# Kernel optimization log

Measured on AMD Instinct MI355X. Metric: run time of the kernel, lower is better.

## Reference

```python
import jax, jax.numpy as jnp
import numpy as np

EPS = 1e-5

def _bn(x, p):
    # eval-mode BatchNorm over the last (channel) axis; p = [gamma, beta, mean, var]
    g, b, m, v = p[0], p[1], p[2], p[3]
    return (x - m) * jax.lax.rsqrt(v + EPS) * g + b

def _mk_bn(key, c):
    kg, kb, km, kv = jax.random.split(key, 4)
    return jnp.stack([
        jax.random.uniform(kg, (c,), minval=0.5, maxval=1.5),
        jax.random.normal(kb, (c,)) * 0.1,
        jax.random.normal(km, (c,)) * 0.1,
        jax.random.uniform(kv, (c,), minval=0.5, maxval=1.5),
    ]).astype(jnp.float32)

def setup_inputs() -> dict:
    key = jax.random.key(0)
    ks = jax.random.split(key, 12)
    B, N, K = 2, 65536, 16
    IN_CH, OUT_CH = 32, 128
    D = IN_CH + 3            # 35
    C16 = OUT_CH // 16       # 8
    C4 = OUT_CH // 4         # 32
    G = 1                    # num_group
    feats = jax.random.normal(ks[0], (B, N, D), dtype=jnp.float32)
    idx = jax.random.randint(ks[1], (B, N, K), 0, N, dtype=jnp.int64)
    s = lambda fi, fo: (2.0 / fi) ** 0.5
    return {
        "features": feats,
        "idx": idx,
        "point_W": jax.random.normal(ks[2], (10, C16), dtype=jnp.float32) * s(10, C16),
        "point_bn": _mk_bn(ks[3], C16),
        "eta_W": jax.random.normal(ks[4], (IN_CH, C16), dtype=jnp.float32) * s(IN_CH, C16),
        "eta_bn": _mk_bn(ks[5], C16),
        "mu_W": jax.random.normal(ks[6], (IN_CH, C16), dtype=jnp.float32) * s(IN_CH, C16),
        "mu_bn": _mk_bn(ks[7], C16),
        "gamma_W": jax.random.normal(ks[8], (D, C4), dtype=jnp.float32) * s(D, C4),
        "gamma_bn": _mk_bn(ks[9], C4),
        "map_W": jax.random.normal(ks[10], (3 * C16, G), dtype=jnp.float32) * s(3 * C16, G),
        "map_bn": _mk_bn(ks[10], G),
        "fc_W": jax.random.normal(ks[11], (C4, OUT_CH), dtype=jnp.float32) * s(C4, OUT_CH),
    }

def reference(features, idx, point_W, point_bn, eta_W, eta_bn, mu_W, mu_bn,
              gamma_W, gamma_bn, map_W, map_bn, fc_W):
    # features: [B,N,D] (D = 3 xyz + in_channel), idx: [B,N,K] kNN indices
    nbr = jax.vmap(lambda f, i: f[i])(features, idx)     # [B,N,K,D] gather
    pn = nbr[..., :3]                                    # neighbor xyz
    pnf = nbr[..., 3:]                                   # neighbor feats
    feat = features[..., 3:]                             # center feats [B,N,Cin]
    p = features[:, :, None, :3]                         # center xyz, bcast over K
    diff = p - pn
    point = jnp.concatenate([
        jnp.sum(diff * diff, axis=-1, keepdims=True),
        jnp.broadcast_to(p, pn.shape), pn, diff,
    ], axis=-1)                                          # [B,N,K,10]
    point = jax.nn.relu(_bn(point @ point_W, point_bn))  # [B,N,K,C16]
    eta = _bn((feat @ eta_W)[:, :, None, :], eta_bn)     # [B,N,1,C16] (repeat over K)
    mu = _bn(pnf @ mu_W, mu_bn)                          # [B,N,K,C16]
    feature = jnp.concatenate([jnp.broadcast_to(eta, mu.shape), mu], axis=-1)  # concat mode
    feature = jnp.concatenate([point, feature], axis=-1)                       # [B,N,K,3*C16]
    feature = jax.nn.relu(_bn(feature @ map_W, map_bn))  # [B,N,K,G]
    gam = _bn(nbr @ gamma_W, gamma_bn)                   # [B,N,K,C4]
    rep = gam.shape[-1] // feature.shape[-1]             # out/4 / num_group
    feature = jnp.tile(feature, (1, 1, 1, rep))          # channel repeat
    out = jnp.max(feature * gam, axis=2)                 # max over neighbors -> [B,N,C4]
    return out @ fc_W                                    # [B,N,out_channel]
```

## Files before the change

### kernel.cpp

```cpp
#include <hip/hip_runtime.h>
#include <hip/hip_fp16.h>
#include <math.h>

#define N_PTS   65536
#define BATCH   2
#define TOTAL   (BATCH * N_PTS)
#define NPACK   24
#define CPACK   12
#define EPSB    1e-5f

typedef short short8 __attribute__((ext_vector_type(8)));
typedef float f32x4 __attribute__((ext_vector_type(4)));

static __device__ inline short f2bf(float x) {
    union { float f; unsigned u; } c; c.f = x;
    unsigned r = c.u + 0x7FFF + ((c.u >> 16) & 1);
    return (short)(r >> 16);
}
static __device__ inline unsigned pk_mul(unsigned a, unsigned b) {
    unsigned r; asm("v_pk_mul_f16 %0, %1, %2" : "=v"(r) : "v"(a), "v"(b)); return r;
}
static __device__ inline unsigned pk_max(unsigned a, unsigned b) {
    unsigned r; asm("v_pk_max_f16 %0, %1, %2" : "=v"(r) : "v"(a), "v"(b)); return r;
}

__global__ __launch_bounds__(256) void k1_precompute(
    const float* __restrict__ feats,
    const float* __restrict__ pW,
    const float* __restrict__ pBN,
    const float* __restrict__ eW,
    const float* __restrict__ eBN,
    const float* __restrict__ mW,
    const float* __restrict__ mBN,
    const float* __restrict__ gW,
    const float* __restrict__ gBN,
    const float* __restrict__ mapW,
    float* __restrict__ packN,
    float* __restrict__ packC)
{
    __shared__ float sF[256 * 35];

    const int tid = threadIdx.x;
    const int base = blockIdx.x * 256;

#pragma unroll
    for (int t = 0; t < 35; ++t)
        sF[t * 256 + tid] = feats[(size_t)base * 35 + t * 256 + tid];
    __syncthreads();

    const float* f = sF + tid * 35;
    const float x = f[0], y = f[1], z = f[2];
    const float pp = x * x + y * y + z * z;

    float G[32];
#pragma unroll
    for (int q = 0; q < 32; ++q) G[q] = 0.f;
#pragma unroll 4
    for (int d = 0; d < 35; ++d) {
        const float fd = f[d];
        const float4* w4 = (const float4*)(gW + d * 32);
#pragma unroll
        for (int q4 = 0; q4 < 8; ++q4) {
            const float4 w = w4[q4];
            G[q4 * 4 + 0] = fmaf(fd, w.x, G[q4 * 4 + 0]);
            G[q4 * 4 + 1] = fmaf(fd, w.y, G[q4 * 4 + 1]);
            G[q4 * 4 + 2] = fmaf(fd, w.z, G[q4 * 4 + 2]);
            G[q4 * 4 + 3] = fmaf(fd, w.w, G[q4 * 4 + 3]);
        }
    }
#pragma unroll
    for (int q = 0; q < 32; ++q) {
        const float g = gBN[q], b = gBN[32 + q], m = gBN[64 + q], v = gBN[96 + q];
        const float s = g / sqrtf(v + EPSB);
        G[q] = fmaf(G[q], s, b - m * s);
    }

    float eta[8], mu[8];
#pragma unroll
    for (int q = 0; q < 8; ++q) { eta[q] = 0.f; mu[q] = 0.f; }
#pragma unroll 4
    for (int i = 0; i < 32; ++i) {
        const float fi = f[3 + i];
        const float4* e4 = (const float4*)(eW + i * 8);
        const float4* m4 = (const float4*)(mW + i * 8);
#pragma unroll
        for (int h = 0; h < 2; ++h) {
            const float4 we = e4[h], wm = m4[h];
            eta[h * 4 + 0] = fmaf(fi, we.x, eta[h * 4 + 0]);
            eta[h * 4 + 1] = fmaf(fi, we.y, eta[h * 4 + 1]);
            eta[h * 4 + 2] = fmaf(fi, we.z, eta[h * 4 + 2]);
            eta[h * 4 + 3] = fmaf(fi, we.w, eta[h * 4 + 3]);
            mu[h * 4 + 0] = fmaf(fi, wm.x, mu[h * 4 + 0]);
            mu[h * 4 + 1] = fmaf(fi, wm.y, mu[h * 4 + 1]);
            mu[h * 4 + 2] = fmaf(fi, wm.z, mu[h * 4 + 2]);
            mu[h * 4 + 3] = fmaf(fi, wm.w, mu[h * 4 + 3]);
        }
    }
    float etadot = 0.f, Mdot = 0.f;
#pragma unroll
    for (int q = 0; q < 8; ++q) {
        const float ge = eBN[q], be = eBN[8 + q], me = eBN[16 + q], ve = eBN[24 + q];
        const float se = ge / sqrtf(ve + EPSB);
        etadot = fmaf(fmaf(eta[q], se, be - me * se), mapW[8 + q], etadot);
        const float gm = mBN[q], bm = mBN[8 + q], mm = mBN[16 + q], vm = mBN[24 + q];
        const float sm = gm / sqrtf(vm + EPSB);
        Mdot = fmaf(fmaf(mu[q], sm, bm - mm * sm), mapW[16 + q], Mdot);
    }

    float Bnp[8], Ap[8];
#pragma unroll
    for (int q = 0; q < 8; ++q) {
        const float pw0 = pW[q];
        const float g = pBN[q], b = pBN[8 + q], m = pBN[16 + q], v = pBN[24 + q];
        const float s = g / sqrtf(v + EPSB);
        const float t = b - m * s;
        const float Braw = pp * pw0
            + x * (pW[32 + q] - pW[56 + q])
            + y * (pW[40 + q] - pW[64 + q])
            + z * (pW[48 + q] - pW[72 + q]);
        const float Araw = pp * pw0
            + x * (pW[8 + q]  + pW[56 + q])
            + y * (pW[16 + q] + pW[64 + q])
            + z * (pW[24 + q] + pW[72 + q]);
        Bnp[q] = Braw * s;
        Ap[q]  = fmaf(Araw, s, t);
    }

    const int j = base + tid;
    float4* PN = (float4*)(packN + (size_t)j * NPACK);
    PN[0] = make_float4(x, y, z, Mdot);
    {
        float4 b4;
        __half2* hb = (__half2*)&b4;
        hb[0] = __floats2half2_rn(Bnp[0], Bnp[1]);
        hb[1] = __floats2half2_rn(Bnp[2], Bnp[3]);
        hb[2] = __floats2half2_rn(Bnp[4], Bnp[5]);
        hb[3] = __floats2half2_rn(Bnp[6], Bnp[7]);
        PN[1] = b4;
    }
#pragma unroll
    for (int q = 0; q < 4; ++q) {
        float4 g4;
        __half2* hg = (__half2*)&g4;
        hg[0] = __floats2half2_rn(G[q * 8 + 0], G[q * 8 + 1]);
        hg[1] = __floats2half2_rn(G[q * 8 + 2], G[q * 8 + 3]);
        hg[2] = __floats2half2_rn(G[q * 8 + 4], G[q * 8 + 5]);
        hg[3] = __floats2half2_rn(G[q * 8 + 6], G[q * 8 + 7]);
        PN[2 + q] = g4;
    }

    float4* PC = (float4*)(packC + (size_t)j * CPACK);
    PC[0] = make_float4(x, y, z, etadot);
    PC[1] = make_float4(Ap[0], Ap[1], Ap[2], Ap[3]);
    PC[2] = make_float4(Ap[4], Ap[5], Ap[6], Ap[7]);
}

__global__ __launch_bounds__(256) void k2_aggregate_fc(
    const int* __restrict__ idx,
    const float* __restrict__ packN,
    const float* __restrict__ packC,
    const float* __restrict__ pW,
    const float* __restrict__ pBN,
    const float* __restrict__ mapW,
    const float* __restrict__ mapBN,
    const float* __restrict__ fcW,
    float* __restrict__ out)
{
    __shared__ __align__(16) unsigned short sPool[32 * 40];

    const int tid  = threadIdx.x;
    const int cl   = tid >> 3;
    const int ks   = tid & 7;
    const int cbase = blockIdx.x * 32;
    const int c    = cbase + cl;
    const int lane = tid & 63;
    const int w    = tid >> 6;
    const int lm   = lane & 15, lq = lane >> 4;

    short8 bfrag[2];
#pragma unroll
    for (int ntj = 0; ntj < 2; ++ntj) {
        const int nt = 2 * w + ntj;
#pragma unroll
        for (int j = 0; j < 8; ++j)
            bfrag[ntj][j] = f2bf(fcW[(8 * lq + j) * 128 + nt * 16 + lm]);
    }

    float ms, mt;
    {
        const float g = mapBN[0], b = mapBN[1], m = mapBN[2], v = mapBN[3];
        ms = g / sqrtf(v + EPSB);
        mt = b - m * ms;
    }
    float W0p[8], mW0[8];
#pragma unroll
    for (int q = 0; q < 8; ++q) {
        const float g = pBN[q], v = pBN[24 + q];
        const float s = g / sqrtf(v + EPSB);
        W0p[q] = 2.f * pW[q] * s;
        mW0[q] = mapW[q];
    }

    const float4* PC = (const float4*)(packC + (size_t)c * CPACK);
    const float4 c0 = PC[0], c1 = PC[1], c2 = PC[2];
    const float px = c0.x, py = c0.y, pz = c0.z, etadot = c0.w;
    const float Ap[8] = { c1.x, c1.y, c1.z, c1.w, c2.x, c2.y, c2.z, c2.w };

    const int2 ib2 = ((const int2*)idx)[c * 8 + ks];
    const int nbr[2] = { ib2.x, ib2.y };
    const int bbase = c & ~(N_PTS - 1);

    unsigned o16[16];
#pragma unroll
    for (int q = 0; q < 16; ++q) o16[q] = 0xFC00FC00u;

#pragma unroll
    for (int k = 0; k < 2; ++k) {
        const int gj = bbase + nbr[k];
        const float4* P = (const float4*)(packN + (size_t)gj * NPACK);
        const float4 h  = P[0];
        const float4 b4 = P[1];
        const float4 g0 = P[2], g1 = P[3], g2 = P[4], g3 = P[5];

        const float dot3 = px * h.x + py * h.y + pz * h.z;
        const __half2* hb = (const __half2*)&b4;
        float pd = 0.f;
#pragma unroll
        for (int q = 0; q < 4; ++q) {
            const float2 bn2 = __half22float2(hb[q]);
            const float u0 = Ap[2 * q]     + bn2.x - dot3 * W0p[2 * q];
            const float u1 = Ap[2 * q + 1] + bn2.y - dot3 * W0p[2 * q + 1];
            pd = fmaf(fmaxf(u0, 0.f), mW0[2 * q], pd);
            pd = fmaf(fmaxf(u1, 0.f), mW0[2 * q + 1], pd);
        }
        float s = fmaf(pd + etadot + h.w, ms, mt);
        s = fmaxf(s, 0.f);

        const unsigned short su = __half_as_ushort(__float2half_rn(s));
        const unsigned s2 = (unsigned)su * 0x10001u;

        const float4 gs[4] = { g0, g1, g2, g3 };
#pragma unroll
        for (int q = 0; q < 4; ++q) {
            const unsigned* hg = (const unsigned*)&gs[q];
#pragma unroll
            for (int r = 0; r < 4; ++r)
                o16[q * 4 + r] = pk_max(o16[q * 4 + r], pk_mul(s2, hg[r]));
        }
    }

#pragma unroll
    for (int q = 0; q < 16; ++q) {
        unsigned v = o16[q];
        v = pk_max(v, (unsigned)__shfl_xor((int)v, 1));
        v = pk_max(v, (unsigned)__shfl_xor((int)v, 2));
        v = pk_max(v, (unsigned)__shfl_xor((int)v, 4));
        o16[q] = v;
    }

    {
        const unsigned v0 = o16[2 * ks], v1 = o16[2 * ks + 1];
        const float c0f = __half2float(__ushort_as_half((unsigned short)(v0 & 0xffff)));
        const float c1f = __half2float(__ushort_as_half((unsigned short)(v0 >> 16)));
        const float c2f = __half2float(__ushort_as_half((unsigned short)(v1 & 0xffff)));
        const float c3f = __half2float(__ushort_as_half((unsigned short)(v1 >> 16)));
        uint2 pk;
        pk.x = (unsigned short)f2bf(c0f) | ((unsigned)(unsigned short)f2bf(c1f) << 16);
        pk.y = (unsigned short)f2bf(c2f) | ((unsigned)(unsigned short)f2bf(c3f) << 16);
        *(uint2*)(sPool + cl * 40 + ks * 4) = pk;
    }
    __syncthreads();

    f32x4 acc[2][2];
#pragma unroll
    for (int a = 0; a < 2; ++a)
#pragma unroll
        for (int b = 0; b < 2; ++b)
            acc[a][b] = (f32x4){0.f, 0.f, 0.f, 0.f};

#pragma unroll
    for (int mtile = 0; mtile < 2; ++mtile) {
        const short8 afrag = *(const short8*)(sPool + (mtile * 16 + lm) * 40 + lq * 8);
#pragma unroll
        for (int ntj = 0; ntj < 2; ++ntj)
            acc[mtile][ntj] = __builtin_amdgcn_mfma_f32_16x16x32_bf16(
                afrag, bfrag[ntj], acc[mtile][ntj], 0, 0, 0);
    }

#pragma unroll
    for (int mtile = 0; mtile < 2; ++mtile)
#pragma unroll
        for (int ntj = 0; ntj < 2; ++ntj) {
            const int nt = 2 * w + ntj;
#pragma unroll
            for (int r = 0; r < 4; ++r)
                out[(size_t)(cbase + mtile * 16 + lq * 4 + r) * 128 + nt * 16 + lm] =
                    acc[mtile][ntj][r];
        }
}

extern "C" void kernel_launch(void* const* d_in, const int* in_sizes, int n_in,
                              void* d_out, int out_size, void* d_ws, size_t ws_size,
                              hipStream_t stream) {
    const float* feats    = (const float*)d_in[0];
    const int*   idx      = (const int*)  d_in[1];
    const float* point_W  = (const float*)d_in[2];
    const float* point_bn = (const float*)d_in[3];
    const float* eta_W    = (const float*)d_in[4];
    const float* eta_bn   = (const float*)d_in[5];
    const float* mu_W     = (const float*)d_in[6];
    const float* mu_bn    = (const float*)d_in[7];
    const float* gamma_W  = (const float*)d_in[8];
    const float* gamma_bn = (const float*)d_in[9];
    const float* map_W    = (const float*)d_in[10];
    const float* map_bn   = (const float*)d_in[11];
    const float* fc_W     = (const float*)d_in[12];
    float* out = (float*)d_out;

    float* packN  = (float*)d_ws;
    float* packC  = packN + (size_t)TOTAL * NPACK;

    hipLaunchKernelGGL(k1_precompute, dim3(TOTAL / 256), dim3(256), 0, stream,
                       feats, point_W, point_bn, eta_W, eta_bn, mu_W, mu_bn,
                       gamma_W, gamma_bn, map_W, packN, packC);
    hipLaunchKernelGGL(k2_aggregate_fc, dim3(TOTAL / 32), dim3(256), 0, stream,
                       idx, packN, packC, point_W, point_bn, map_W, map_bn,
                       fc_W, out);
}
```

Baseline: 177.0 us.

## Quantize gathered gamma to int8, pack neighbor record in 64B, remap blocks per XCD

Shrinks the per-neighbor packed record from 96 to 64 bytes. It stores xyz and the point terms as fp16 and the 32 gamma values as per-point-scaled int8, which cuts gather traffic in the aggregation kernel. It also remaps block IDs so each XCD works on one batch half, giving the random gathers better L2 locality. It switches the pooled values and fc MFMA from bf16 to fp16 to drop conversions, uses nontemporal output stores, and stages weights in LDS in the precompute kernel. Risks include int8 quantization error, fp16 xyz precision loss, and extra dequantization ALU work.

```diff
diff --git a/kernel.cpp b/kernel.cpp
--- a/kernel.cpp
+++ b/kernel.cpp
@@ -5,20 +5,19 @@
 #define N_PTS   65536
 #define BATCH   2
 #define TOTAL   (BATCH * N_PTS)
-#define NPACK   24
+#define NPACK_DW 16
 #define CPACK   12
 #define EPSB    1e-5f
 
-typedef short short8 __attribute__((ext_vector_type(8)));
-typedef float f32x4 __attribute__((ext_vector_type(4)));
-
-static __device__ inline short f2bf(float x) {
-    union { float f; unsigned u; } c; c.f = x;
-    unsigned r = c.u + 0x7FFF + ((c.u >> 16) & 1);
-    return (short)(r >> 16);
-}
-static __device__ inline unsigned pk_mul(unsigned a, unsigned b) {
-    unsigned r; asm("v_pk_mul_f16 %0, %1, %2" : "=v"(r) : "v"(a), "v"(b)); return r;
+typedef float  f32x4  __attribute__((ext_vector_type(4)));
+typedef _Float16 f16x8 __attribute__((ext_vector_type(8)));
+
+static __device__ inline unsigned h2u(float a, float b) {
+    __half2 h = __floats2half2_rn(a, b);
+    union { __half2 h; unsigned u; } cv; cv.h = h; return cv.u;
+}
+static __device__ inline float2 u2f2(unsigned u) {
+    union { unsigned u; __half2 h; } cv; cv.u = u; return __half22float2(cv.h);
 }
 static __device__ inline unsigned pk_max(unsigned a, unsigned b) {
     unsigned r; asm("v_pk_max_f16 %0, %1, %2" : "=v"(r) : "v"(a), "v"(b)); return r;
@@ -35,14 +34,19 @@
     const float* __restrict__ gW,
     const float* __restrict__ gBN,
     const float* __restrict__ mapW,
-    float* __restrict__ packN,
+    unsigned* __restrict__ packN,
     float* __restrict__ packC)
 {
+    __shared__ float sG[35 * 32];
+    __shared__ float sE[32 * 8];
+    __shared__ float sM[32 * 8];
     __shared__ float sF[256 * 35];
 
     const int tid = threadIdx.x;
     const int base = blockIdx.x * 256;
 
+    for (int i = tid; i < 35 * 32; i += 256) sG[i] = gW[i];
+    sE[tid] = eW[tid]; sM[tid] = mW[tid];
 #pragma unroll
     for (int t = 0; t < 35; ++t)
         sF[t * 256 + tid] = feats[(size_t)base * 35 + t * 256 + tid];
@@ -58,7 +62,7 @@
 #pragma unroll 4
     for (int d = 0; d < 35; ++d) {
         const float fd = f[d];
-        const float4* w4 = (const float4*)(gW + d * 32);
+        const float4* w4 = (const float4*)(sG + d * 32);
 #pragma unroll
         for (int q4 = 0; q4 < 8; ++q4) {
             const float4 w = w4[q4];
@@ -81,8 +85,8 @@
 #pragma unroll 4
     for (int i = 0; i < 32; ++i) {
         const float fi = f[3 + i];
-        const float4* e4 = (const float4*)(eW + i * 8);
-        const float4* m4 = (const float4*)(mW + i * 8);
+        const float4* e4 = (const float4*)(sE + i * 8);
+        const float4* m4 = (const float4*)(sM + i * 8);
 #pragma unroll
         for (int h = 0; h < 2; ++h) {
             const float4 we = e4[h], wm = m4[h];
@@ -127,27 +131,28 @@
     }
 
     const int j = base + tid;
-    float4* PN = (float4*)(packN + (size_t)j * NPACK);
-    PN[0] = make_float4(x, y, z, Mdot);
-    {
-        float4 b4;
-        __half2* hb = (__half2*)&b4;
-        hb[0] = __floats2half2_rn(Bnp[0], Bnp[1]);
-        hb[1] = __floats2half2_rn(Bnp[2], Bnp[3]);
-        hb[2] = __floats2half2_rn(Bnp[4], Bnp[5]);
-        hb[3] = __floats2half2_rn(Bnp[6], Bnp[7]);
-        PN[1] = b4;
-    }
-#pragma unroll
-    for (int q = 0; q < 4; ++q) {
-        float4 g4;
-        __half2* hg = (__half2*)&g4;
-        hg[0] = __floats2half2_rn(G[q * 8 + 0], G[q * 8 + 1]);
-        hg[1] = __floats2half2_rn(G[q * 8 + 2], G[q * 8 + 3]);
-        hg[2] = __floats2half2_rn(G[q * 8 + 4], G[q * 8 + 5]);
-        hg[3] = __floats2half2_rn(G[q * 8 + 6], G[q * 8 + 7]);
-        PN[2 + q] = g4;
-    }
+    float gmax = 0.f;
+#pragma unroll
+    for (int q = 0; q < 32; ++q) gmax = fmaxf(gmax, fabsf(G[q]));
+    const float inv = (gmax > 0.f) ? (127.f / gmax) : 0.f;
+    unsigned gq[8];
+#pragma unroll
+    for (int qd = 0; qd < 8; ++qd) {
+        unsigned d = 0;
+#pragma unroll
+        for (int b = 0; b < 4; ++b) {
+            const int q8 = (int)rintf(G[4 * qd + b] * inv) + 128;
+            d |= ((unsigned)q8 & 0xffu) << (8 * b);
+        }
+        gq[qd] = d;
+    }
+    union { float f; unsigned u; } sc; sc.f = gmax;
+
+    uint4* PN = (uint4*)(packN + (size_t)j * NPACK_DW);
+    PN[0] = make_uint4(h2u(x, y), h2u(z, Mdot), h2u(Bnp[0], Bnp[1]), h2u(Bnp[2], Bnp[3]));
+    PN[1] = make_uint4(h2u(Bnp[4], Bnp[5]), h2u(Bnp[6], Bnp[7]), gq[0], gq[1]);
+    PN[2] = make_uint4(gq[2], gq[3], gq[4], gq[5]);
+    PN[3] = make_uint4(gq[6], gq[7], sc.u, 0u);
 
     float4* PC = (float4*)(packC + (size_t)j * CPACK);
     PC[0] = make_float4(x, y, z, etadot);
@@ -157,7 +162,7 @@
 
 __global__ __launch_bounds__(256) void k2_aggregate_fc(
     const int* __restrict__ idx,
-    const float* __restrict__ packN,
+    const unsigned* __restrict__ packN,
     const float* __restrict__ packC,
     const float* __restrict__ pW,
     const float* __restrict__ pBN,
@@ -168,22 +173,29 @@
 {
     __shared__ __align__(16) unsigned short sPool[32 * 40];
 
+    const int bid  = blockIdx.x;
+    const int xcd  = bid & 7, slot = bid >> 3;
+    const int cb   = (xcd < 4) ? (slot * 4 + xcd)
+                               : (2048 + slot * 4 + (xcd - 4));
+    const int cbase = cb * 32;
+
     const int tid  = threadIdx.x;
     const int cl   = tid >> 3;
     const int ks   = tid & 7;
-    const int cbase = blockIdx.x * 32;
     const int c    = cbase + cl;
     const int lane = tid & 63;
     const int w    = tid >> 6;
     const int lm   = lane & 15, lq = lane >> 4;
 
-    short8 bfrag[2];
+    f16x8 bfrag[2];
 #pragma unroll
     for (int ntj = 0; ntj < 2; ++ntj) {
         const int nt = 2 * w + ntj;
+        union { unsigned short u[8]; f16x8 v; } cv;
 #pragma unroll
         for (int j = 0; j < 8; ++j)
-            bfrag[ntj][j] = f2bf(fcW[(8 * lq + j) * 128 + nt * 16 + lm]);
+            cv.u[j] = __half_as_ushort(__float2half_rn(fcW[(8 * lq + j) * 128 + nt * 16 + lm]));
+        bfrag[ntj] = cv.v;
     }
 
     float ms, mt;
@@ -207,45 +219,51 @@
     const float Ap[8] = { c1.x, c1.y, c1.z, c1.w, c2.x, c2.y, c2.z, c2.w };
 
     const int2 ib2 = ((const int2*)idx)[c * 8 + ks];
-    const int nbr[2] = { ib2.x, ib2.y };
     const int bbase = c & ~(N_PTS - 1);
 
     unsigned o16[16];
 #pragma unroll
     for (int q = 0; q < 16; ++q) o16[q] = 0xFC00FC00u;
 
+    const uint4* P0 = (const uint4*)(packN + (size_t)(bbase + ib2.x) * NPACK_DW);
+    const uint4* P1 = (const uint4*)(packN + (size_t)(bbase + ib2.y) * NPACK_DW);
+    uint4 n0[4] = { P0[0], P0[1], P0[2], P0[3] };
+    uint4 n1[4] = { P1[0], P1[1], P1[2], P1[3] };
+
 #pragma unroll
     for (int k = 0; k < 2; ++k) {
-        const int gj = bbase + nbr[k];
-        const float4* P = (const float4*)(packN + (size_t)gj * NPACK);
-        const float4 h  = P[0];
-        const float4 b4 = P[1];
-        const float4 g0 = P[2], g1 = P[3], g2 = P[4], g3 = P[5];
-
-        const float dot3 = px * h.x + py * h.y + pz * h.z;
-        const __half2* hb = (const __half2*)&b4;
+        const uint4* N = k ? n1 : n0;
+        const float2 xy = u2f2(N[0].x), zM = u2f2(N[0].y);
+        const float dot3 = px * xy.x + py * xy.y + pz * zM.x;
+
+        const unsigned bn[4] = { N[0].z, N[0].w, N[1].x, N[1].y };
         float pd = 0.f;
 #pragma unroll
         for (int q = 0; q < 4; ++q) {
-            const float2 bn2 = __half22float2(hb[q]);
+            const float2 bn2 = u2f2(bn[q]);
             const float u0 = Ap[2 * q]     + bn2.x - dot3 * W0p[2 * q];
             const float u1 = Ap[2 * q + 1] + bn2.y - dot3 * W0p[2 * q + 1];
             pd = fmaf(fmaxf(u0, 0.f), mW0[2 * q], pd);
             pd = fmaf(fmaxf(u1, 0.f), mW0[2 * q + 1], pd);
         }
-        float s = fmaf(pd + etadot + h.w, ms, mt);
+        float s = fmaf(pd + etadot + zM.y, ms, mt);
         s = fmaxf(s, 0.f);
 
-        const unsigned short su = __half_as_ushort(__float2half_rn(s));
-        const unsigned s2 = (unsigned)su * 0x10001u;
-
-        const float4 gs[4] = { g0, g1, g2, g3 };
-#pragma unroll
-        for (int q = 0; q < 4; ++q) {
-            const unsigned* hg = (const unsigned*)&gs[q];
-#pragma unroll
-            for (int r = 0; r < 4; ++r)
-                o16[q * 4 + r] = pk_max(o16[q * 4 + r], pk_mul(s2, hg[r]));
+        union { unsigned u; float f; } sc; sc.u = N[3].z;
+        const float t  = s * sc.f * (1.f / 127.f);
+        const float nt = -128.f * t;
+
+        const unsigned gd[8] = { N[1].z, N[1].w, N[2].x, N[2].y,
+                                 N[2].z, N[2].w, N[3].x, N[3].y };
+#pragma unroll
+        for (int qd = 0; qd < 8; ++qd) {
+            const unsigned dwv = gd[qd];
+            const float v0 = fmaf(t, (float)( dwv        & 0xffu), nt);
+            const float v1 = fmaf(t, (float)((dwv >>  8) & 0xffu), nt);
+            const float v2 = fmaf(t, (float)((dwv >> 16) & 0xffu), nt);
+            const float v3 = fmaf(t, (float)( dwv >> 24        ), nt);
+            o16[2 * qd]     = pk_max(o16[2 * qd],     h2u(v0, v1));
+            o16[2 * qd + 1] = pk_max(o16[2 * qd + 1], h2u(v2, v3));
         }
     }
 
@@ -259,14 +277,9 @@
     }
 
     {
-        const unsigned v0 = o16[2 * ks], v1 = o16[2 * ks + 1];
-        const float c0f = __half2float(__ushort_as_half((unsigned short)(v0 & 0xffff)));
-        const float c1f = __half2float(__ushort_as_half((unsigned short)(v0 >> 16)));
-        const float c2f = __half2float(__ushort_as_half((unsigned short)(v1 & 0xffff)));
-        const float c3f = __half2float(__ushort_as_half((unsigned short)(v1 >> 16)));
         uint2 pk;
-        pk.x = (unsigned short)f2bf(c0f) | ((unsigned)(unsigned short)f2bf(c1f) << 16);
-        pk.y = (unsigned short)f2bf(c2f) | ((unsigned)(unsigned short)f2bf(c3f) << 16);
+        pk.x = o16[2 * ks];
+        pk.y = o16[2 * ks + 1];
         *(uint2*)(sPool + cl * 40 + ks * 4) = pk;
     }
     __syncthreads();
@@ -280,10 +293,10 @@
 
 #pragma unroll
     for (int mtile = 0; mtile < 2; ++mtile) {
-        const short8 afrag = *(const short8*)(sPool + (mtile * 16 + lm) * 40 + lq * 8);
+        const f16x8 afrag = *(const f16x8*)(sPool + (mtile * 16 + lm) * 40 + lq * 8);
 #pragma unroll
         for (int ntj = 0; ntj < 2; ++ntj)
-            acc[mtile][ntj] = __builtin_amdgcn_mfma_f32_16x16x32_bf16(
+            acc[mtile][ntj] = __builtin_amdgcn_mfma_f32_16x16x32_f16(
                 afrag, bfrag[ntj], acc[mtile][ntj], 0, 0, 0);
     }
 
@@ -294,8 +307,8 @@
             const int nt = 2 * w + ntj;
 #pragma unroll
             for (int r = 0; r < 4; ++r)
-                out[(size_t)(cbase + mtile * 16 + lq * 4 + r) * 128 + nt * 16 + lm] =
-                    acc[mtile][ntj][r];
+                __builtin_nontemporal_store(acc[mtile][ntj][r],
+                    &out[(size_t)(cbase + mtile * 16 + lq * 4 + r) * 128 + nt * 16 + lm]);
         }
 }
 
@@ -317,8 +330,8 @@
     const float* fc_W     = (const float*)d_in[12];
     float* out = (float*)d_out;
 
-    float* packN  = (float*)d_ws;
-    float* packC  = packN + (size_t)TOTAL * NPACK;
+    unsigned* packN = (unsigned*)d_ws;
+    float*    packC = (float*)(packN + (size_t)TOTAL * NPACK_DW);
 
     hipLaunchKernelGGL(k1_precompute, dim3(TOTAL / 256), dim3(256), 0, stream,
                        feats, point_W, point_bn, eta_W, eta_bn, mu_W, mu_bn,
```

Measured after the change: 161.5 us. 8.8% less time.
